# Kernel tuning notes

Measured on AMD Instinct MI355X. Metric: run time of the kernel, lower is better.

Reference implementation:

```python
import jax, jax.numpy as jnp
import numpy as np

E, R, CIN, COUT = 8, 8, 256, 256
B, H, W = 16, 64, 64
DN = ('NCHW', 'OIHW', 'NCHW')


def setup_inputs() -> dict:
    key = jax.random.key(0)
    k1, k2, k3, k4 = jax.random.split(key, 4)
    x = jax.random.normal(k1, (B, CIN, H, W), jnp.float32)
    probs = jax.nn.softmax(jax.random.normal(k2, (E,), jnp.float32))
    # in conv: rank filters over in_channels, kernel (1,3); out conv: kernel (3,1)
    weight_in = jax.random.normal(k3, (E, R, CIN, 1, 3), jnp.float32) * 0.02
    weight_out = jax.random.normal(k4, (E, COUT, R, 3, 1), jnp.float32) * 0.02
    return {"x": x, "probs": probs, "weight_in": weight_in, "weight_out": weight_out}


def _expert_conv(x, w_in, w_out):
    # in conv: stride (1,1), padding (0,1) -> [B,R,H,W]
    h = jax.lax.conv_general_dilated(x, w_in, window_strides=(1, 1),
                                     padding=[(0, 0), (1, 1)], dimension_numbers=DN)
    # out conv: stride (1,1), padding (1,0) -> [B,COUT,H,W]
    return jax.lax.conv_general_dilated(h, w_out, window_strides=(1, 1),
                                        padding=[(1, 1), (0, 0)], dimension_numbers=DN)


def reference(x, probs, weight_in, weight_out):
    # vmap over experts replaces the Python loop; outs: [E,B,COUT,H,W]
    outs = jax.vmap(lambda wi, wo: _expert_conv(x, wi, wo))(weight_in, weight_out)
    # probability-weighted sum over experts (stack + sum in the original)
    return jnp.einsum('e,ebchw->bchw', probs, outs)
```

## Files before the change

kernel.cpp:

```cpp
#include <hip/hip_runtime.h>
#include <hip/hip_bf16.h>


typedef __bf16 bf16x8 __attribute__((ext_vector_type(8)));
typedef __bf16 bf16x4 __attribute__((ext_vector_type(4)));
typedef float  f32x4  __attribute__((ext_vector_type(4)));

#define CIN_  256
#define COUT_ 256
#define M1    64
#define K1    768
#define K2    192
#define CS    264
#define HS    200

static __device__ __forceinline__ unsigned short f2bf(float f) {
    union { float f; unsigned u; } v; v.f = f;
    unsigned r = v.u + 0x7FFFu + ((v.u >> 16) & 1u);
    return (unsigned short)(r >> 16);
}

__global__ void prep_weights(const float* __restrict__ probs,
                             const float* __restrict__ w_in,
                             const float* __restrict__ w_out,
                             unsigned short* __restrict__ W1,
                             unsigned short* __restrict__ W2,
                             unsigned short* __restrict__ hT) {
    int idx = blockIdx.x * blockDim.x + threadIdx.x;
    if (idx < M1 * K1) {
        int er = idx / K1, rem = idx % K1;
        int kx = rem / CIN_, c = rem % CIN_;
        int e = er >> 3;
        W1[idx] = f2bf(probs[e] * w_in[(er * CIN_ + c) * 3 + kx]);
    } else if (idx < 2 * M1 * K1) {
        int i2 = idx - M1 * K1;
        int o = i2 / K2, rem = i2 % K2;
        int ky = rem / M1, er = rem % M1;
        int e = er >> 3, r = er & 7;
        W2[i2] = f2bf(w_out[((e * COUT_ + o) * 8 + r) * 3 + ky]);
    } else {
        int i3 = idx - 2 * M1 * K1;
        if (i3 < 16384) {
            int b = i3 >> 10, r = i3 & 1023;
            int yp = (r >> 9) * 65;
            int col = (r & 511) * 8;
            bf16x8 z = {};
            *(bf16x8*)(hT + ((b * 66 + yp) * 4096) + col) = z;
        }
    }
}

__global__ __launch_bounds__(256, 4)
void conv_in_kernel(const float* __restrict__ x,
                    const unsigned short* __restrict__ W1,
                    unsigned short* __restrict__ hT) {
    __shared__ unsigned short xs[66 * CS];
    const int bid  = blockIdx.x;
    const int b    = bid >> 6, y = bid & 63;
    const int tid  = threadIdx.x;
    const int lane = tid & 63;
    const int wave = tid >> 6;
    const int g    = lane >> 4;
    const int lr   = lane & 15;

    if (tid < 66) {
        int row = (tid < 33) ? 0 : 65;
        int col = (tid - (tid < 33 ? 0 : 33)) * 8;
        bf16x4 z4 = {};
        *(bf16x4*)&xs[row * CS + col] = z4;
        *(bf16x4*)&xs[row * CS + col + 4] = z4;
    }

    const int crow = tid >> 4;
    const int n4   = (tid & 15) << 2;
    const int swzt = (tid & 7) << 3;
    const float* xbase = x + ((b * CIN_ + crow) * 64 + y) * 64 + n4;
    unsigned short* wr = &xs[(n4 + 1) * CS];

    #pragma unroll
    for (int r = 0; r < 4; ++r) {
        float4 ld[4];
        #pragma unroll
        for (int q = 0; q < 4; ++q)
            ld[q] = *(const float4*)(xbase + (r * 4 + q) * 16 * 4096);
        #pragma unroll
        for (int q = 0; q < 4; ++q) {
            int cx = ((r * 4 + q) * 16 + crow) ^ swzt;
            wr[0 * CS + cx] = f2bf(ld[q].x);
            wr[1 * CS + cx] = f2bf(ld[q].y);
            wr[2 * CS + cx] = f2bf(ld[q].z);
            wr[3 * CS + cx] = f2bf(ld[q].w);
        }
    }
    __syncthreads();

    f32x4 acc[4];
    #pragma unroll
    for (int i = 0; i < 4; ++i) acc[i] = (f32x4){0.f, 0.f, 0.f, 0.f};

    const unsigned short* w1p = W1 + (wave * 16 + lr) * K1 + g * 8;
    #pragma unroll
    for (int kx = 0; kx < 3; ++kx) {
        bf16x8 af[8];
        #pragma unroll
        for (int cc = 0; cc < 8; ++cc)
            af[cc] = *(const bf16x8*)(w1p + kx * CIN_ + cc * 32);
        int ns0 = lr + kx;
        int sz0 = (((ns0 - 1) >> 2) & 7) << 3;
        int ns1 = ns0 + 16, sz1 = (((ns1 - 1) >> 2) & 7) << 3;
        int ns2 = ns0 + 32, sz2 = (((ns2 - 1) >> 2) & 7) << 3;
        int ns3 = ns0 + 48, sz3 = (((ns3 - 1) >> 2) & 7) << 3;
        const unsigned short* r0 = &xs[ns0 * CS];
        const unsigned short* r1 = &xs[ns1 * CS];
        const unsigned short* r2p = &xs[ns2 * CS];
        const unsigned short* r3 = &xs[ns3 * CS];
        #pragma unroll
        for (int cc = 0; cc < 8; ++cc) {
            int co = cc * 32 + g * 8;
            acc[0] = __builtin_amdgcn_mfma_f32_16x16x32_bf16(
                af[cc], *(const bf16x8*)&r0[co ^ sz0], acc[0], 0, 0, 0);
            acc[1] = __builtin_amdgcn_mfma_f32_16x16x32_bf16(
                af[cc], *(const bf16x8*)&r1[co ^ sz1], acc[1], 0, 0, 0);
            acc[2] = __builtin_amdgcn_mfma_f32_16x16x32_bf16(
                af[cc], *(const bf16x8*)&r2p[co ^ sz2], acc[2], 0, 0, 0);
            acc[3] = __builtin_amdgcn_mfma_f32_16x16x32_bf16(
                af[cc], *(const bf16x8*)&r3[co ^ sz3], acc[3], 0, 0, 0);
        }
    }
    unsigned short* hp = hT + ((b * 66 + y + 1) * 64) * 64;
    #pragma unroll
    for (int nt = 0; nt < 4; ++nt) {
        int n = nt * 16 + lr;
        bf16x4 pk;
        #pragma unroll
        for (int r2 = 0; r2 < 4; ++r2) pk[r2] = (__bf16)acc[nt][r2];
        *(bf16x4*)&hp[n * 64 + wave * 16 + g * 4] = pk;
    }
}

__global__ __launch_bounds__(256, 4)
void conv_out_kernel(const unsigned short* __restrict__ hT,
                     const unsigned short* __restrict__ W2,
                     float* __restrict__ out) {
    __shared__ unsigned short hs[64 * HS];
    const int bid  = blockIdx.x;
    const int b    = bid >> 6, y = bid & 63;
    const int tid  = threadIdx.x;
    const int lane = tid & 63;
    const int wave = tid >> 6;
    const int g    = lane >> 4;
    const int lr   = lane & 15;

    const int rrow = tid >> 3;
    const int u8   = (tid & 7) * 8;
    #pragma unroll
    for (int v = 0; v < 6; ++v) {
        int R  = v * 32 + rrow;
        int ky = R >> 6, xr = R & 63;
        const unsigned short* src = hT + (((b * 66) + y + ky) * 64 + xr) * 64 + u8;
        *(bf16x8*)&hs[xr * HS + ky * 64 + u8] = *(const bf16x8*)src;
    }
    __syncthreads();

    f32x4 acc[4][4];
    #pragma unroll
    for (int ot = 0; ot < 4; ++ot)
        #pragma unroll
        for (int nt = 0; nt < 4; ++nt) acc[ot][nt] = (f32x4){0.f, 0.f, 0.f, 0.f};

    #pragma unroll
    for (int kc = 0; kc < 6; ++kc) {
        bf16x8 bfrag[4];
        #pragma unroll
        for (int nt = 0; nt < 4; ++nt)
            bfrag[nt] = *(const bf16x8*)&hs[(nt * 16 + lr) * HS + kc * 32 + g * 8];
        #pragma unroll
        for (int ot = 0; ot < 4; ++ot) {
            bf16x8 af = *(const bf16x8*)(W2 + ((wave * 4 + ot) * 16 + lr) * K2 +
                                         kc * 32 + g * 8);
            #pragma unroll
            for (int nt = 0; nt < 4; ++nt)
                acc[ot][nt] = __builtin_amdgcn_mfma_f32_16x16x32_bf16(af, bfrag[nt],
                                                                      acc[ot][nt], 0, 0, 0);
        }
    }

    #pragma unroll
    for (int ot = 0; ot < 4; ++ot) {
        #pragma unroll
        for (int r2 = 0; r2 < 4; ++r2) {
            int o = (wave * 4 + ot) * 16 + g * 4 + r2;
            float* orow = out + ((b * COUT_ + o) * 64 + y) * 64;
            #pragma unroll
            for (int nt = 0; nt < 4; ++nt)
                orow[nt * 16 + lr] = acc[ot][nt][r2];
        }
    }
}

extern "C" void kernel_launch(void* const* d_in, const int* in_sizes, int n_in,
                              void* d_out, int out_size, void* d_ws, size_t ws_size,
                              hipStream_t stream) {
    const float* x     = (const float*)d_in[0];
    const float* probs = (const float*)d_in[1];
    const float* w_in  = (const float*)d_in[2];
    const float* w_out = (const float*)d_in[3];
    float* out = (float*)d_out;

    unsigned short* W1 = (unsigned short*)d_ws;
    unsigned short* W2 = W1 + M1 * K1;
    unsigned short* hT = W2 + COUT_ * K2;

    prep_weights<<<(2 * M1 * K1 + 16384 + 255) / 256, 256, 0, stream>>>(
        probs, w_in, w_out, W1, W2, hT);
    conv_in_kernel<<<16 * 64, 256, 0, stream>>>(x, W1, hT);
    conv_out_kernel<<<16 * 64, 256, 0, stream>>>(hT, W2, out);
}
```

Before: 56.66 us.

## Fuse in-conv and out-conv into one kernel with LDS-resident intermediate

Merges the two convolution kernels into a single kernel where each block computes four rows of the rank intermediate (two output rows plus halo) into swizzled LDS, then runs the out-conv from LDS. This removes the global hT round trip, its zero-padding setup, and one launch, and keeps W1/W2 fragments in registers. In exchange, the first conv is recomputed for halo rows and x is loaded twice per output row. The grid also halves, with a lower occupancy bound and larger register and LDS footprint.

```diff
diff --git a/kernel.cpp b/kernel.cpp
--- a/kernel.cpp
+++ b/kernel.cpp
@@ -12,7 +12,7 @@
 #define K1    768
 #define K2    192
 #define CS    264
-#define HS    200
+#define HS2   264
 
 static __device__ __forceinline__ unsigned short f2bf(float f) {
     union { float f; unsigned u; } v; v.f = f;
@@ -24,44 +24,47 @@
                              const float* __restrict__ w_in,
                              const float* __restrict__ w_out,
                              unsigned short* __restrict__ W1,
-                             unsigned short* __restrict__ W2,
-                             unsigned short* __restrict__ hT) {
+                             unsigned short* __restrict__ W2) {
     int idx = blockIdx.x * blockDim.x + threadIdx.x;
     if (idx < M1 * K1) {
         int er = idx / K1, rem = idx % K1;
         int kx = rem / CIN_, c = rem % CIN_;
         int e = er >> 3;
         W1[idx] = f2bf(probs[e] * w_in[(er * CIN_ + c) * 3 + kx]);
-    } else if (idx < 2 * M1 * K1) {
+    } else {
         int i2 = idx - M1 * K1;
         int o = i2 / K2, rem = i2 % K2;
         int ky = rem / M1, er = rem % M1;
         int e = er >> 3, r = er & 7;
         W2[i2] = f2bf(w_out[((e * COUT_ + o) * 8 + r) * 3 + ky]);
-    } else {
-        int i3 = idx - 2 * M1 * K1;
-        if (i3 < 16384) {
-            int b = i3 >> 10, r = i3 & 1023;
-            int yp = (r >> 9) * 65;
-            int col = (r & 511) * 8;
-            bf16x8 z = {};
-            *(bf16x8*)(hT + ((b * 66 + yp) * 4096) + col) = z;
-        }
-    }
-}
-
-__global__ __launch_bounds__(256, 4)
-void conv_in_kernel(const float* __restrict__ x,
-                    const unsigned short* __restrict__ W1,
-                    unsigned short* __restrict__ hT) {
+    }
+}
+
+__global__ __launch_bounds__(256, 2)
+void fused_kernel(const float* __restrict__ x,
+                  const unsigned short* __restrict__ W1,
+                  const unsigned short* __restrict__ W2,
+                  float* __restrict__ out) {
     __shared__ unsigned short xs[66 * CS];
+    __shared__ unsigned short hs[64 * HS2];
     const int bid  = blockIdx.x;
-    const int b    = bid >> 6, y = bid & 63;
+    const int b    = bid >> 5;
+    const int y0   = (bid & 31) << 1;
     const int tid  = threadIdx.x;
     const int lane = tid & 63;
     const int wave = tid >> 6;
     const int g    = lane >> 4;
     const int lr   = lane & 15;
+
+    bf16x8 w1f[3][8];
+    {
+        const unsigned short* w1p = W1 + (wave * 16 + lr) * K1 + g * 8;
+        #pragma unroll
+        for (int kx = 0; kx < 3; ++kx)
+            #pragma unroll
+            for (int cc = 0; cc < 8; ++cc)
+                w1f[kx][cc] = *(const bf16x8*)(w1p + kx * CIN_ + cc * 32);
+    }
 
     if (tid < 66) {
         int row = (tid < 33) ? 0 : 65;
@@ -74,126 +77,118 @@
     const int crow = tid >> 4;
     const int n4   = (tid & 15) << 2;
     const int swzt = (tid & 7) << 3;
-    const float* xbase = x + ((b * CIN_ + crow) * 64 + y) * 64 + n4;
-    unsigned short* wr = &xs[(n4 + 1) * CS];
-
-    #pragma unroll
-    for (int r = 0; r < 4; ++r) {
-        float4 ld[4];
-        #pragma unroll
-        for (int q = 0; q < 4; ++q)
-            ld[q] = *(const float4*)(xbase + (r * 4 + q) * 16 * 4096);
-        #pragma unroll
-        for (int q = 0; q < 4; ++q) {
-            int cx = ((r * 4 + q) * 16 + crow) ^ swzt;
-            wr[0 * CS + cx] = f2bf(ld[q].x);
-            wr[1 * CS + cx] = f2bf(ld[q].y);
-            wr[2 * CS + cx] = f2bf(ld[q].z);
-            wr[3 * CS + cx] = f2bf(ld[q].w);
+
+    for (int yy = 0; yy < 4; ++yy) {
+        const int y = y0 - 1 + yy;
+        const bool yok = ((unsigned)y < 64u);
+        __syncthreads();
+        const float* xbase = x + ((b * CIN_ + crow) * 64 + (yok ? y : 0)) * 64 + n4;
+        unsigned short* wr = &xs[(n4 + 1) * CS];
+        #pragma unroll
+        for (int r = 0; r < 4; ++r) {
+            float4 ld[4];
+            if (yok) {
+                #pragma unroll
+                for (int q = 0; q < 4; ++q)
+                    ld[q] = *(const float4*)(xbase + (r * 4 + q) * 16 * 4096);
+            } else {
+                #pragma unroll
+                for (int q = 0; q < 4; ++q) ld[q] = make_float4(0.f, 0.f, 0.f, 0.f);
+            }
+            #pragma unroll
+            for (int q = 0; q < 4; ++q) {
+                int cx = ((r * 4 + q) * 16 + crow) ^ swzt;
+                wr[0 * CS + cx] = f2bf(ld[q].x);
+                wr[1 * CS + cx] = f2bf(ld[q].y);
+                wr[2 * CS + cx] = f2bf(ld[q].z);
+                wr[3 * CS + cx] = f2bf(ld[q].w);
+            }
+        }
+        __syncthreads();
+
+        f32x4 acc[4];
+        #pragma unroll
+        for (int i = 0; i < 4; ++i) acc[i] = (f32x4){0.f, 0.f, 0.f, 0.f};
+        #pragma unroll
+        for (int kx = 0; kx < 3; ++kx) {
+            int ns0 = lr + kx;
+            int sz0 = (((ns0 - 1) >> 2) & 7) << 3;
+            int ns1 = ns0 + 16, sz1 = (((ns1 - 1) >> 2) & 7) << 3;
+            int ns2 = ns0 + 32, sz2 = (((ns2 - 1) >> 2) & 7) << 3;
+            int ns3 = ns0 + 48, sz3 = (((ns3 - 1) >> 2) & 7) << 3;
+            const unsigned short* r0  = &xs[ns0 * CS];
+            const unsigned short* r1  = &xs[ns1 * CS];
+            const unsigned short* r2p = &xs[ns2 * CS];
+            const unsigned short* r3  = &xs[ns3 * CS];
+            #pragma unroll
+            for (int cc = 0; cc < 8; ++cc) {
+                int co = cc * 32 + g * 8;
+                acc[0] = __builtin_amdgcn_mfma_f32_16x16x32_bf16(
+                    w1f[kx][cc], *(const bf16x8*)&r0[co ^ sz0], acc[0], 0, 0, 0);
+                acc[1] = __builtin_amdgcn_mfma_f32_16x16x32_bf16(
+                    w1f[kx][cc], *(const bf16x8*)&r1[co ^ sz1], acc[1], 0, 0, 0);
+                acc[2] = __builtin_amdgcn_mfma_f32_16x16x32_bf16(
+                    w1f[kx][cc], *(const bf16x8*)&r2p[co ^ sz2], acc[2], 0, 0, 0);
+                acc[3] = __builtin_amdgcn_mfma_f32_16x16x32_bf16(
+                    w1f[kx][cc], *(const bf16x8*)&r3[co ^ sz3], acc[3], 0, 0, 0);
+            }
+        }
+        #pragma unroll
+        for (int nt = 0; nt < 4; ++nt) {
+            int n = nt * 16 + lr;
+            bf16x4 pk;
+            #pragma unroll
+            for (int r2 = 0; r2 < 4; ++r2) pk[r2] = (__bf16)acc[nt][r2];
+            int col = (yy * 64 + wave * 16 + g * 4) ^ ((n & 7) << 3);
+            *(bf16x4*)&hs[n * HS2 + col] = pk;
         }
     }
     __syncthreads();
 
-    f32x4 acc[4];
-    #pragma unroll
-    for (int i = 0; i < 4; ++i) acc[i] = (f32x4){0.f, 0.f, 0.f, 0.f};
-
-    const unsigned short* w1p = W1 + (wave * 16 + lr) * K1 + g * 8;
-    #pragma unroll
-    for (int kx = 0; kx < 3; ++kx) {
-        bf16x8 af[8];
-        #pragma unroll
-        for (int cc = 0; cc < 8; ++cc)
-            af[cc] = *(const bf16x8*)(w1p + kx * CIN_ + cc * 32);
-        int ns0 = lr + kx;
-        int sz0 = (((ns0 - 1) >> 2) & 7) << 3;
-        int ns1 = ns0 + 16, sz1 = (((ns1 - 1) >> 2) & 7) << 3;
-        int ns2 = ns0 + 32, sz2 = (((ns2 - 1) >> 2) & 7) << 3;
-        int ns3 = ns0 + 48, sz3 = (((ns3 - 1) >> 2) & 7) << 3;
-        const unsigned short* r0 = &xs[ns0 * CS];
-        const unsigned short* r1 = &xs[ns1 * CS];
-        const unsigned short* r2p = &xs[ns2 * CS];
-        const unsigned short* r3 = &xs[ns3 * CS];
-        #pragma unroll
-        for (int cc = 0; cc < 8; ++cc) {
-            int co = cc * 32 + g * 8;
-            acc[0] = __builtin_amdgcn_mfma_f32_16x16x32_bf16(
-                af[cc], *(const bf16x8*)&r0[co ^ sz0], acc[0], 0, 0, 0);
-            acc[1] = __builtin_amdgcn_mfma_f32_16x16x32_bf16(
-                af[cc], *(const bf16x8*)&r1[co ^ sz1], acc[1], 0, 0, 0);
-            acc[2] = __builtin_amdgcn_mfma_f32_16x16x32_bf16(
-                af[cc], *(const bf16x8*)&r2p[co ^ sz2], acc[2], 0, 0, 0);
-            acc[3] = __builtin_amdgcn_mfma_f32_16x16x32_bf16(
-                af[cc], *(const bf16x8*)&r3[co ^ sz3], acc[3], 0, 0, 0);
-        }
-    }
-    unsigned short* hp = hT + ((b * 66 + y + 1) * 64) * 64;
-    #pragma unroll
-    for (int nt = 0; nt < 4; ++nt) {
-        int n = nt * 16 + lr;
-        bf16x4 pk;
-        #pragma unroll
-        for (int r2 = 0; r2 < 4; ++r2) pk[r2] = (__bf16)acc[nt][r2];
-        *(bf16x4*)&hp[n * 64 + wave * 16 + g * 4] = pk;
-    }
-}
-
-__global__ __launch_bounds__(256, 4)
-void conv_out_kernel(const unsigned short* __restrict__ hT,
-                     const unsigned short* __restrict__ W2,
-                     float* __restrict__ out) {
-    __shared__ unsigned short hs[64 * HS];
-    const int bid  = blockIdx.x;
-    const int b    = bid >> 6, y = bid & 63;
-    const int tid  = threadIdx.x;
-    const int lane = tid & 63;
-    const int wave = tid >> 6;
-    const int g    = lane >> 4;
-    const int lr   = lane & 15;
-
-    const int rrow = tid >> 3;
-    const int u8   = (tid & 7) * 8;
-    #pragma unroll
-    for (int v = 0; v < 6; ++v) {
-        int R  = v * 32 + rrow;
-        int ky = R >> 6, xr = R & 63;
-        const unsigned short* src = hT + (((b * 66) + y + ky) * 64 + xr) * 64 + u8;
-        *(bf16x8*)&hs[xr * HS + ky * 64 + u8] = *(const bf16x8*)src;
-    }
-    __syncthreads();
-
-    f32x4 acc[4][4];
+    bf16x8 w2f[4][6];
     #pragma unroll
     for (int ot = 0; ot < 4; ++ot)
         #pragma unroll
-        for (int nt = 0; nt < 4; ++nt) acc[ot][nt] = (f32x4){0.f, 0.f, 0.f, 0.f};
+        for (int kc = 0; kc < 6; ++kc)
+            w2f[ot][kc] = *(const bf16x8*)(W2 + ((wave * 4 + ot) * 16 + lr) * K2 +
+                                           kc * 32 + g * 8);
 
     #pragma unroll
-    for (int kc = 0; kc < 6; ++kc) {
-        bf16x8 bfrag[4];
-        #pragma unroll
-        for (int nt = 0; nt < 4; ++nt)
-            bfrag[nt] = *(const bf16x8*)&hs[(nt * 16 + lr) * HS + kc * 32 + g * 8];
+    for (int ry = 0; ry < 2; ++ry) {
+        f32x4 acc2[4][4];
+        #pragma unroll
+        for (int ot = 0; ot < 4; ++ot)
+            #pragma unroll
+            for (int nt = 0; nt < 4; ++nt) acc2[ot][nt] = (f32x4){0.f, 0.f, 0.f, 0.f};
+
+        #pragma unroll
+        for (int kc = 0; kc < 6; ++kc) {
+            bf16x8 bfrag[4];
+            #pragma unroll
+            for (int nt = 0; nt < 4; ++nt) {
+                int n = nt * 16 + lr;
+                int col = (ry * 64 + kc * 32 + g * 8) ^ ((n & 7) << 3);
+                bfrag[nt] = *(const bf16x8*)&hs[n * HS2 + col];
+            }
+            #pragma unroll
+            for (int ot = 0; ot < 4; ++ot)
+                #pragma unroll
+                for (int nt = 0; nt < 4; ++nt)
+                    acc2[ot][nt] = __builtin_amdgcn_mfma_f32_16x16x32_bf16(
+                        w2f[ot][kc], bfrag[nt], acc2[ot][nt], 0, 0, 0);
+        }
+
+        const int yo = y0 + ry;
         #pragma unroll
         for (int ot = 0; ot < 4; ++ot) {
-            bf16x8 af = *(const bf16x8*)(W2 + ((wave * 4 + ot) * 16 + lr) * K2 +
-                                         kc * 32 + g * 8);
-            #pragma unroll
-            for (int nt = 0; nt < 4; ++nt)
-                acc[ot][nt] = __builtin_amdgcn_mfma_f32_16x16x32_bf16(af, bfrag[nt],
-                                                                      acc[ot][nt], 0, 0, 0);
-        }
-    }
-
-    #pragma unroll
-    for (int ot = 0; ot < 4; ++ot) {
-        #pragma unroll
-        for (int r2 = 0; r2 < 4; ++r2) {
-            int o = (wave * 4 + ot) * 16 + g * 4 + r2;
-            float* orow = out + ((b * COUT_ + o) * 64 + y) * 64;
-            #pragma unroll
-            for (int nt = 0; nt < 4; ++nt)
-                orow[nt * 16 + lr] = acc[ot][nt][r2];
+            #pragma unroll
+            for (int r2 = 0; r2 < 4; ++r2) {
+                int o = (wave * 4 + ot) * 16 + g * 4 + r2;
+                float* orow = out + ((b * COUT_ + o) * 64 + yo) * 64;
+                #pragma unroll
+                for (int nt = 0; nt < 4; ++nt)
+                    orow[nt * 16 + lr] = acc2[ot][nt][r2];
+            }
         }
     }
 }
@@ -209,10 +204,7 @@
 
     unsigned short* W1 = (unsigned short*)d_ws;
     unsigned short* W2 = W1 + M1 * K1;
-    unsigned short* hT = W2 + COUT_ * K2;
-
-    prep_weights<<<(2 * M1 * K1 + 16384 + 255) / 256, 256, 0, stream>>>(
-        probs, w_in, w_out, W1, W2, hT);
-    conv_in_kernel<<<16 * 64, 256, 0, stream>>>(x, W1, hT);
-    conv_out_kernel<<<16 * 64, 256, 0, stream>>>(hT, W2, out);
-}
+
+    prep_weights<<<384, 256, 0, stream>>>(probs, w_in, w_out, W1, W2);
+    fused_kernel<<<16 * 32, 256, 0, stream>>>(x, W1, W2, out);
+}
```

Measured after the change: 49.25 us. 13.1% less time.
